# Performance work log

Hardware: AMD Instinct MI355X
Metric: run time of the kernel (lower is better)

Reference implementation:

```python
import jax, jax.numpy as jnp
import numpy as np

L = 3          # num_layer
E_DIM = 64     # emb_dim
B = 4          # graphs per batch
N = 20000      # nodes per graph
E = 320000     # edges per graph
IN_DIM = 21    # raw node feature dim (Linear(21, emb_dim))
BN_EPS = 1e-5


def setup_inputs() -> dict:
    key = jax.random.key(0)
    ks = jax.random.split(key, 16)
    h2 = 2 * E_DIM
    inp = {
        "x": jax.random.normal(ks[0], (B, N, IN_DIM), dtype=jnp.float32),
        "edge_index": jax.random.randint(ks[1], (B, 2, E), 0, N, dtype=jnp.int64),
        "edge_attr": jax.random.normal(ks[2], (B, E, 1), dtype=jnp.float32),
        # layer-0 input node embedding Linear(21, emb)
        "inW": jax.random.normal(ks[3], (IN_DIM, E_DIM), dtype=jnp.float32) * 0.1,
        "inb": jnp.zeros((E_DIM,), dtype=jnp.float32),
        # per-layer edge encoder Linear(1, emb)
        "edgeW": jax.random.normal(ks[4], (L, 1, E_DIM), dtype=jnp.float32) * 0.1,
        "edgeb": jnp.zeros((L, E_DIM), dtype=jnp.float32),
        # per-layer MLP: Linear(2e,2e) -> BN(2e) -> ReLU -> Linear(2e,e)
        "W1": jax.random.normal(ks[5], (L, h2, h2), dtype=jnp.float32) * 0.05,
        "b1": jnp.zeros((L, h2), dtype=jnp.float32),
        "gamma": jnp.ones((L, h2), dtype=jnp.float32),
        "beta": jnp.zeros((L, h2), dtype=jnp.float32),
        "W2": jax.random.normal(ks[6], (L, h2, E_DIM), dtype=jnp.float32) * 0.05,
        "b2": jnp.zeros((L, E_DIM), dtype=jnp.float32),
    }
    return inp


def _batchnorm_train(h, g, b):
    # BatchNorm1d in training mode: per-graph stats over the node dim, biased var
    m = h.mean(axis=0)
    v = jnp.mean((h - m) ** 2, axis=0)
    return (h - m) * jax.lax.rsqrt(v + BN_EPS) * g + b


def _gin_layer(xg, eig, eag, W1l, b1l, gl, bel, W2l, b2l):
    # xg [N,e], eig [2,E], eag [E,e]
    x_j = xg[eig[0]]                                   # gather source nodes [E,e]
    msg = jnp.concatenate([x_j, eag], axis=-1)         # [E,2e]
    aggr = jax.ops.segment_sum(msg, eig[1], num_segments=N)  # scatter-add [N,2e]
    h = aggr @ W1l + b1l
    h = _batchnorm_train(h, gl, bel)
    h = jax.nn.relu(h)
    return h @ W2l + b2l                               # [N,e]


def reference(x, edge_index, edge_attr, inW, inb, edgeW, edgeb, W1, b1, gamma, beta, W2, b2):
    h = x
    for l in range(L):
        ea = edge_attr @ edgeW[l] + edgeb[l]           # [B,E,e] edge embeddings
        if l == 0:
            h = h @ inW + inb                          # [B,N,e]
        h = jax.vmap(_gin_layer, in_axes=(0, 0, 0, None, None, None, None, None, None))(
            h, edge_index, ea, W1[l], b1[l], gamma[l], beta[l], W2[l], b2[l])
        if l < L - 1:                                  # drop_ratio=0 -> dropout is identity
            h = jax.nn.relu(h)
    return h  # JK='last'
```

## Files before the change

kernel.cpp:

```cpp
#include <hip/hip_runtime.h>
#include <hip/hip_bf16.h>
#include <hip/hip_fp16.h>

#define NB 4
#define NN 20000
#define NE 320000
#define IND 21
#define ED 64
#define H2 128
#define CAP 48
#define NRANGE 32
#define RNODES 625
#define BINCAP 160
#define SCAP 11264
#define BN_EPS 1e-5f

typedef __attribute__((ext_vector_type(8))) short bf16x8;
typedef __attribute__((ext_vector_type(4))) float f32x4;

__device__ __forceinline__ short f2bf(float f) {
    unsigned u = __float_as_uint(f);
    u += 0x7fffu + ((u >> 16) & 1u);
    return (short)(u >> 16);
}

__device__ __forceinline__ void add8(float* ac, const uint4 rv) {
    const float2 f0 = __half22float2(*(const __half2*)&rv.x);
    const float2 f1 = __half22float2(*(const __half2*)&rv.y);
    const float2 f2 = __half22float2(*(const __half2*)&rv.z);
    const float2 f3 = __half22float2(*(const __half2*)&rv.w);
    ac[0] += f0.x; ac[1] += f0.y; ac[2] += f1.x; ac[3] += f1.y;
    ac[4] += f2.x; ac[5] += f2.y; ac[6] += f3.x; ac[7] += f3.y;
}


__global__ __launch_bounds__(256) void k_compact(
    const int* __restrict__ ei, const float* __restrict__ eattr,
    uint2* __restrict__ stage, int* __restrict__ rcnt)
{
    __shared__ uint2 bins[NRANGE][BINCAP];
    __shared__ int lcnt[NRANGE];
    __shared__ int lbase[NRANGE];
    const int b = blockIdx.y;
    const int e0 = blockIdx.x * 2048;
    const int tid = threadIdx.x;
    if (tid < NRANGE) lcnt[tid] = 0;
    __syncthreads();
    const int* srcp = ei + (size_t)b * 2 * NE;
    const int* dstp = srcp + NE;
    const float* ap = eattr + (size_t)b * NE;
    #pragma unroll
    for (int it = 0; it < 8; ++it) {
        const int e = e0 + it * 256 + tid;
        if (e < NE) {
            const int dst = dstp[e];
            const int src = srcp[e];
            const float a = ap[e];
            const int r = dst / RNODES;
            const unsigned lo = ((unsigned)src & 0xffffu) | (__float_as_uint(a) & 0xffff0000u);
            const int p = atomicAdd(&lcnt[r], 1);
            if (p < BINCAP) bins[r][p] = make_uint2(lo, (unsigned)dst);
        }
    }
    __syncthreads();
    if (tid < NRANGE) lbase[tid] = atomicAdd(&rcnt[b * NRANGE + tid], min(lcnt[tid], BINCAP));
    __syncthreads();
    for (int r = 0; r < NRANGE; ++r) {
        const int c = min(lcnt[r], BINCAP);
        uint2* dstg = stage + (size_t)(b * NRANGE + r) * SCAP + lbase[r];
        for (int i = tid; i < c; i += 256) dstg[i] = bins[r][i];
    }
}

__global__ __launch_bounds__(256) void k_scatter(
    const uint2* __restrict__ stage, const int* __restrict__ rcnt,
    int* __restrict__ cnt, unsigned int* __restrict__ bucket)
{
    const int b = blockIdx.x >> 5;
    const int g = blockIdx.x & 31;
    const int count = min(rcnt[b * NRANGE + g], SCAP);
    const uint2* st = stage + (size_t)(b * NRANGE + g) * SCAP;
    for (int idx = threadIdx.x; idx < count; idx += 256) {
        const uint2 rec = st[idx];
        const int node = b * NN + (int)rec.y;
        const int p = atomicAdd(&cnt[node], 1);
        if (p < CAP) bucket[(size_t)node * CAP + p] = rec.x;
    }
}

__global__ __launch_bounds__(256) void k_in(
    const float* __restrict__ x, const float* __restrict__ inW,
    const float* __restrict__ inb, __half* __restrict__ h)
{
    const int b = blockIdx.y;
    const int t = blockIdx.x * 256 + threadIdx.x;
    const int n = t >> 6;
    const int c = t & 63;
    if (n >= NN) return;
    const float* xr = x + ((size_t)b * NN + n) * IND;
    float acc = inb[c];
    #pragma unroll
    for (int k = 0; k < IND; ++k) acc += xr[k] * inW[k * ED + c];
    h[((size_t)b * NN + n) * ED + c] = __float2half(acc);
}

__global__ __launch_bounds__(256) void k_prep(
    const float* __restrict__ W1, const float* __restrict__ W2,
    const float* __restrict__ edgeW, const float* __restrict__ edgeb,
    short* __restrict__ W1T, short* __restrict__ W2T,
    float* __restrict__ uv_all, float* __restrict__ stats_all)
{
    const int l = blockIdx.x;
    const int tid = threadIdx.x;
    ((float4*)(stats_all + l * 1024))[tid] = make_float4(0.f, 0.f, 0.f, 0.f);
    for (int i = tid; i < H2 * ED; i += 256) {
        const int j = i >> 6, k = i & 63;
        W1T[l * 8192 + i] = f2bf(W1[(size_t)l * H2 * H2 + k * H2 + j]);
    }
    for (int i = tid; i < ED * H2; i += 256) {
        const int c = i >> 7, k = i & 127;
        W2T[l * 8192 + i] = f2bf(W2[(size_t)l * H2 * ED + k * ED + c]);
    }
    if (tid < H2) {
        float u = 0.f, v = 0.f;
        for (int k = 0; k < ED; ++k) {
            const float w = W1[(size_t)l * H2 * H2 + (ED + k) * H2 + tid];
            u += edgeW[l * ED + k] * w;
            v += edgeb[l * ED + k] * w;
        }
        uv_all[l * 256 + tid] = u;
        uv_all[l * 256 + H2 + tid] = v;
    }
}


__global__ __launch_bounds__(256) void k_aggr_stats(
    const __half* __restrict__ h, const unsigned int* __restrict__ bucket,
    const int* __restrict__ cnt_arr, const short* __restrict__ W1Tl,
    const float* __restrict__ b1l, const float* __restrict__ uv_l,
    short* __restrict__ aggr_bf, float* __restrict__ s_attr,
    float* __restrict__ stats_l, int write_sattr)
{
    __shared__ short w1t[H2 * 72];
    __shared__ short atb[32 * 72];
    __shared__ float sdl[32], ddl[32];
    __shared__ float uL[H2], vL[H2], bbL[H2];
    const int tid = threadIdx.x;
    const int g = blockIdx.x & 7;
    const int b = g >> 1;
    const int t = ((int)blockIdx.x >> 3) * 2 + (g & 1);
    if (t >= NN / 32) return;
    const int n0 = t * 32;

    for (int i = tid; i < 1024; i += 256)
        *(uint4*)&w1t[(i >> 3) * 72 + (i & 7) * 8] = ((const uint4*)W1Tl)[i];
    if (tid < H2) { uL[tid] = uv_l[tid]; vL[tid] = uv_l[H2 + tid]; bbL[tid] = b1l[tid]; }

    {
        const int node = n0 + (tid >> 3);
        const int q = tid & 7;
        const int cntraw = cnt_arr[b * NN + node];
        const int cnt = min(cntraw, CAP);
        const unsigned int* row = bucket + (size_t)(b * NN + node) * CAP;
        const __half* hp = h + (size_t)b * NN * ED + q * 8;
        float ac[8];
        #pragma unroll
        for (int i = 0; i < 8; ++i) ac[i] = 0.f;
        float sa = 0.f;
        int j = 0;
        for (; j + 4 <= cnt; j += 4) {
            const uint4 ss = *(const uint4*)(row + j);
            const uint4 r0 = *(const uint4*)(hp + (size_t)(ss.x & 0xffffu) * ED);
            const uint4 r1 = *(const uint4*)(hp + (size_t)(ss.y & 0xffffu) * ED);
            const uint4 r2 = *(const uint4*)(hp + (size_t)(ss.z & 0xffffu) * ED);
            const uint4 r3 = *(const uint4*)(hp + (size_t)(ss.w & 0xffffu) * ED);
            sa += __uint_as_float(ss.x & 0xffff0000u) + __uint_as_float(ss.y & 0xffff0000u)
                + __uint_as_float(ss.z & 0xffff0000u) + __uint_as_float(ss.w & 0xffff0000u);
            add8(ac, r0); add8(ac, r1); add8(ac, r2); add8(ac, r3);
        }
        for (; j < cnt; ++j) {
            const unsigned e = row[j];
            sa += __uint_as_float(e & 0xffff0000u);
            const uint4 r0 = *(const uint4*)(hp + (size_t)(e & 0xffffu) * ED);
            add8(ac, r0);
        }
        uint4 pk;
        pk.x = (unsigned short)f2bf(ac[0]) | ((unsigned int)(unsigned short)f2bf(ac[1]) << 16);
        pk.y = (unsigned short)f2bf(ac[2]) | ((unsigned int)(unsigned short)f2bf(ac[3]) << 16);
        pk.z = (unsigned short)f2bf(ac[4]) | ((unsigned int)(unsigned short)f2bf(ac[5]) << 16);
        pk.w = (unsigned short)f2bf(ac[6]) | ((unsigned int)(unsigned short)f2bf(ac[7]) << 16);
        *(uint4*)&atb[(tid >> 3) * 72 + q * 8] = pk;
        *(uint4*)&aggr_bf[((size_t)b * NN + node) * ED + q * 8] = pk;
        if (q == 0) {
            sdl[tid >> 3] = sa;
            ddl[tid >> 3] = (float)cntraw;
            if (write_sattr) s_attr[b * NN + node] = sa;
        }
    }
    __syncthreads();

    const int l = tid & 63;
    const int w = tid >> 6;
    const int m = l & 15, quad = l >> 4;
    const int mt = w & 1;
    const int jb = (w >> 1) * 4;
    f32x4 acc[4];
    #pragma unroll
    for (int i = 0; i < 4; ++i) acc[i] = (f32x4){0.f, 0.f, 0.f, 0.f};
    #pragma unroll
    for (int kc = 0; kc < 2; ++kc) {
        const bf16x8 fa = *(const bf16x8*)&atb[(mt * 16 + m) * 72 + kc * 32 + quad * 8];
        #pragma unroll
        for (int t2 = 0; t2 < 4; ++t2) {
            const bf16x8 fb = *(const bf16x8*)&w1t[((jb + t2) * 16 + m) * 72 + kc * 32 + quad * 8];
            acc[t2] = __builtin_amdgcn_mfma_f32_16x16x32_bf16(fa, fb, acc[t2], 0, 0, 0);
        }
    }
    float sa_r[4], dg_r[4];
    #pragma unroll
    for (int r = 0; r < 4; ++r) {
        const int row = mt * 16 + quad * 4 + r;
        sa_r[r] = sdl[row]; dg_r[r] = ddl[row];
    }
    #pragma unroll
    for (int t2 = 0; t2 < 4; ++t2) {
        const int j = (jb + t2) * 16 + m;
        const float u = uL[j], v = vL[j], bb = bbL[j];
        float ls = 0.f, lq = 0.f;
        #pragma unroll
        for (int r = 0; r < 4; ++r) {
            const float h1 = acc[t2][r] + sa_r[r] * u + dg_r[r] * v + bb;
            ls += h1; lq += h1 * h1;
        }
        ls += __shfl_xor(ls, 16); ls += __shfl_xor(ls, 32);
        lq += __shfl_xor(lq, 16); lq += __shfl_xor(lq, 32);
        if (l < 16) {
            atomicAdd(&stats_l[b * H2 + j], ls);
            atomicAdd(&stats_l[NB * H2 + b * H2 + j], lq);
        }
    }
}

__global__ __launch_bounds__(256) void k_mlp_out(
    const short* __restrict__ aggr_bf, const float* __restrict__ s_attr,
    const int* __restrict__ cnt_arr, const short* __restrict__ W1Tl,
    const short* __restrict__ W2Tl, const float* __restrict__ b1l,
    const float* __restrict__ uv_l, const float* __restrict__ stats_l,
    const float* __restrict__ gamma_l, const float* __restrict__ beta_l,
    const float* __restrict__ b2l, __half* __restrict__ outh,
    float* __restrict__ outf, int last)
{
    __shared__ short wt[H2 * 72];
    __shared__ short ab[64 * 72];
    __shared__ short pb[64 * 136];
    __shared__ float sdl[64], ddl[64];
    __shared__ float uL[H2], vL[H2], bbL[H2], scL[H2], shL[H2];
    const int tid = threadIdx.x;
    const int g = blockIdx.x & 7;
    const int b = g >> 1;
    const int t = ((int)blockIdx.x >> 3) * 2 + (g & 1);
    if (t >= (NN + 63) / 64) return;
    const int n0 = t * 64;

    for (int i = tid; i < 1024; i += 256)
        *(uint4*)&wt[(i >> 3) * 72 + (i & 7) * 8] = ((const uint4*)W1Tl)[i];
    for (int i = tid; i < 512; i += 256)
        *(uint4*)&ab[(i >> 3) * 72 + (i & 7) * 8] =
            ((const uint4*)(aggr_bf + ((size_t)b * NN + n0) * ED))[i];
    if (tid < 64) sdl[tid] = s_attr[b * NN + n0 + tid];
    else if (tid < 128) ddl[tid - 64] = (float)cnt_arr[b * NN + n0 + tid - 64];
    if (tid < H2) {
        const int j = tid;
        const float mm = stats_l[b * H2 + j] * (1.f / NN);
        const float var = fmaxf(stats_l[NB * H2 + b * H2 + j] * (1.f / NN) - mm * mm, 0.f);
        const float rs = rsqrtf(var + BN_EPS);
        const float sc = gamma_l[j] * rs;
        scL[j] = sc;
        shL[j] = beta_l[j] - mm * sc;
        uL[j] = uv_l[j]; vL[j] = uv_l[H2 + j]; bbL[j] = b1l[j];
    }
    __syncthreads();

    const int l = tid & 63;
    const int w = tid >> 6;
    const int m = l & 15, quad = l >> 4;
    {
        f32x4 acc[8];
        #pragma unroll
        for (int i = 0; i < 8; ++i) acc[i] = (f32x4){0.f, 0.f, 0.f, 0.f};
        #pragma unroll
        for (int kc = 0; kc < 2; ++kc) {
            const bf16x8 fa = *(const bf16x8*)&ab[(w * 16 + m) * 72 + kc * 32 + quad * 8];
            #pragma unroll
            for (int t2 = 0; t2 < 8; ++t2) {
                const bf16x8 fb = *(const bf16x8*)&wt[(t2 * 16 + m) * 72 + kc * 32 + quad * 8];
                acc[t2] = __builtin_amdgcn_mfma_f32_16x16x32_bf16(fa, fb, acc[t2], 0, 0, 0);
            }
        }
        float sa_r[4], dg_r[4];
        #pragma unroll
        for (int r = 0; r < 4; ++r) {
            const int row = w * 16 + quad * 4 + r;
            sa_r[r] = sdl[row]; dg_r[r] = ddl[row];
        }
        #pragma unroll
        for (int t2 = 0; t2 < 8; ++t2) {
            const int j = t2 * 16 + m;
            const float u = uL[j], v = vL[j], bb = bbL[j];
            const float sc = scL[j], sh = shL[j];
            #pragma unroll
            for (int r = 0; r < 4; ++r) {
                const float h1 = acc[t2][r] + sa_r[r] * u + dg_r[r] * v + bb;
                pb[(w * 16 + quad * 4 + r) * 136 + j] = f2bf(fmaxf(h1 * sc + sh, 0.f));
            }
        }
    }
    __syncthreads();
    for (int i = tid; i < 1024; i += 256)
        *(uint4*)&wt[(i >> 4) * 136 + (i & 15) * 8] = ((const uint4*)W2Tl)[i];
    __syncthreads();
    {
        f32x4 acc2[4];
        #pragma unroll
        for (int i = 0; i < 4; ++i) acc2[i] = (f32x4){0.f, 0.f, 0.f, 0.f};
        #pragma unroll
        for (int kc = 0; kc < 4; ++kc) {
            const bf16x8 fa = *(const bf16x8*)&pb[(w * 16 + m) * 136 + kc * 32 + quad * 8];
            #pragma unroll
            for (int t2 = 0; t2 < 4; ++t2) {
                const bf16x8 fb = *(const bf16x8*)&wt[(t2 * 16 + m) * 136 + kc * 32 + quad * 8];
                acc2[t2] = __builtin_amdgcn_mfma_f32_16x16x32_bf16(fa, fb, acc2[t2], 0, 0, 0);
            }
        }
        #pragma unroll
        for (int t2 = 0; t2 < 4; ++t2) {
            const int c = t2 * 16 + m;
            const float bb2 = b2l[c];
            #pragma unroll
            for (int r = 0; r < 4; ++r) {
                const int row = w * 16 + quad * 4 + r;
                const int n = n0 + row;
                if (n < NN) {
                    const size_t idx = ((size_t)b * NN + n) * ED + c;
                    float o = acc2[t2][r] + bb2;
                    if (last) outf[idx] = o;
                    else outh[idx] = __float2half(fmaxf(o, 0.f));
                }
            }
        }
    }
}


extern "C" void kernel_launch(void* const* d_in, const int* in_sizes, int n_in,
                              void* d_out, int out_size, void* d_ws, size_t ws_size,
                              hipStream_t stream) {
    const float* x     = (const float*)d_in[0];
    const int*   ei    = (const int*)d_in[1];
    const float* eattr = (const float*)d_in[2];
    const float* inW   = (const float*)d_in[3];
    const float* inb   = (const float*)d_in[4];
    const float* edgeW = (const float*)d_in[5];
    const float* edgeb = (const float*)d_in[6];
    const float* W1    = (const float*)d_in[7];
    const float* b1    = (const float*)d_in[8];
    const float* gamma = (const float*)d_in[9];
    const float* beta  = (const float*)d_in[10];
    const float* W2    = (const float*)d_in[11];
    const float* b2    = (const float*)d_in[12];
    float* out = (float*)d_out;

    float* s_attr = (float*)d_ws;
    int*   cnt    = (int*)(s_attr + NB * NN);
    int*   rcnt   = cnt + NB * NN;
    uint2* stage  = (uint2*)(rcnt + 128);
    unsigned int* bucket = (unsigned int*)(stage + (size_t)NB * NRANGE * SCAP);
    short* aggr_bf = (short*)(bucket + (size_t)NB * NN * CAP);
    __half* hh    = (__half*)(aggr_bf + (size_t)NB * NN * ED);
    short* W1T    = (short*)(hh + (size_t)NB * NN * ED);
    short* W2T    = W1T + 3 * 8192;
    float* uv_all = (float*)(W2T + 3 * 8192);
    float* stats  = uv_all + 3 * 256;

    hipMemsetAsync(cnt, 0, ((size_t)NB * NN + 128) * sizeof(int), stream);

    k_compact<<<dim3((NE + 2047) / 2048, NB), 256, 0, stream>>>(ei, eattr, stage, rcnt);
    k_scatter<<<NB * NRANGE, 256, 0, stream>>>(stage, rcnt, cnt, bucket);
    k_in<<<dim3(NN * ED / 256, NB), 256, 0, stream>>>(x, inW, inb, hh);
    k_prep<<<3, 256, 0, stream>>>(W1, W2, edgeW, edgeb, W1T, W2T, uv_all, stats);

    const int nblk1 = 8 * ((NN / 32 + 1) / 2);
    const int nblk2 = 8 * (((NN + 63) / 64 + 1) / 2);
    for (int l = 0; l < 3; ++l) {
        k_aggr_stats<<<nblk1, 256, 0, stream>>>(hh, bucket, cnt,
            W1T + l * 8192, b1 + l * H2, uv_all + l * 256,
            aggr_bf, s_attr, stats + l * 1024, (l == 0) ? 1 : 0);
        k_mlp_out<<<nblk2, 256, 0, stream>>>(aggr_bf, s_attr, cnt,
            W1T + l * 8192, W2T + l * 8192, b1 + l * H2, uv_all + l * 256,
            stats + l * 1024, gamma + l * H2, beta + l * H2, b2 + l * ED,
            hh, out, (l == 2) ? 1 : 0);
    }
}
```

Measured before the change: 372.7 us.

## Shrink aggregation tiles, split edge lists across threads, read weights directly from global

The aggregation kernel now handles 16 nodes per block instead of 32. It stages each block's bucket rows in shared memory and splits each node's edge list across two half-threads, which are combined with a shuffle. Both kernels stop staging W1/W2 (and aggr rows) in LDS and load MFMA fragments straight from global, removing the staging loops and one barrier. This raises parallelism and memory-level concurrency in the gather, but adds more blocks and repeated global weight reads that rely on the cache.

```diff
diff --git a/kernel.cpp b/kernel.cpp
--- a/kernel.cpp
+++ b/kernel.cpp
@@ -141,95 +141,105 @@
     short* __restrict__ aggr_bf, float* __restrict__ s_attr,
     float* __restrict__ stats_l, int write_sattr)
 {
-    __shared__ short w1t[H2 * 72];
-    __shared__ short atb[32 * 72];
-    __shared__ float sdl[32], ddl[32];
+    __shared__ unsigned int brow[16 * CAP];
+    __shared__ short atb[16 * 72];
+    __shared__ float sdl[16], ddl[16];
     __shared__ float uL[H2], vL[H2], bbL[H2];
     const int tid = threadIdx.x;
     const int g = blockIdx.x & 7;
     const int b = g >> 1;
     const int t = ((int)blockIdx.x >> 3) * 2 + (g & 1);
-    if (t >= NN / 32) return;
-    const int n0 = t * 32;
-
-    for (int i = tid; i < 1024; i += 256)
-        *(uint4*)&w1t[(i >> 3) * 72 + (i & 7) * 8] = ((const uint4*)W1Tl)[i];
+    const int n0 = t * 16;
+
+    const int l = tid & 63;
+    const int w = tid >> 6;
+    const int m = l & 15, quad = l >> 4;
+
+    bf16x8 fb[2][2];
+    #pragma unroll
+    for (int t2 = 0; t2 < 2; ++t2)
+        #pragma unroll
+        for (int kc = 0; kc < 2; ++kc)
+            fb[t2][kc] = *(const bf16x8*)&W1Tl[((w * 2 + t2) * 16 + m) * 64 + kc * 32 + quad * 8];
+
     if (tid < H2) { uL[tid] = uv_l[tid]; vL[tid] = uv_l[H2 + tid]; bbL[tid] = b1l[tid]; }
 
     {
-        const int node = n0 + (tid >> 3);
-        const int q = tid & 7;
-        const int cntraw = cnt_arr[b * NN + node];
+        const unsigned int* bsrc = bucket + (size_t)(b * NN + n0) * CAP;
+        #pragma unroll
+        for (int i = tid; i < 16 * CAP; i += 256) brow[i] = bsrc[i];
+    }
+    __syncthreads();
+
+    {
+        const int node = tid >> 4;
+        const int sub = tid & 15;
+        const int q = sub & 7, eh = sub >> 3;
+        const int cntraw = cnt_arr[b * NN + n0 + node];
         const int cnt = min(cntraw, CAP);
-        const unsigned int* row = bucket + (size_t)(b * NN + node) * CAP;
+        const int hcnt = (cnt + 1) >> 1;
+        const int j1 = eh ? cnt : hcnt;
+        const unsigned int* row = &brow[node * CAP];
         const __half* hp = h + (size_t)b * NN * ED + q * 8;
         float ac[8];
         #pragma unroll
         for (int i = 0; i < 8; ++i) ac[i] = 0.f;
         float sa = 0.f;
-        int j = 0;
-        for (; j + 4 <= cnt; j += 4) {
-            const uint4 ss = *(const uint4*)(row + j);
-            const uint4 r0 = *(const uint4*)(hp + (size_t)(ss.x & 0xffffu) * ED);
-            const uint4 r1 = *(const uint4*)(hp + (size_t)(ss.y & 0xffffu) * ED);
-            const uint4 r2 = *(const uint4*)(hp + (size_t)(ss.z & 0xffffu) * ED);
-            const uint4 r3 = *(const uint4*)(hp + (size_t)(ss.w & 0xffffu) * ED);
-            sa += __uint_as_float(ss.x & 0xffff0000u) + __uint_as_float(ss.y & 0xffff0000u)
-                + __uint_as_float(ss.z & 0xffff0000u) + __uint_as_float(ss.w & 0xffff0000u);
+        int j = eh ? hcnt : 0;
+        for (; j + 4 <= j1; j += 4) {
+            const unsigned e0 = row[j], e1 = row[j + 1], e2 = row[j + 2], e3 = row[j + 3];
+            const uint4 r0 = *(const uint4*)(hp + (size_t)(e0 & 0xffffu) * ED);
+            const uint4 r1 = *(const uint4*)(hp + (size_t)(e1 & 0xffffu) * ED);
+            const uint4 r2 = *(const uint4*)(hp + (size_t)(e2 & 0xffffu) * ED);
+            const uint4 r3 = *(const uint4*)(hp + (size_t)(e3 & 0xffffu) * ED);
+            sa += __uint_as_float(e0 & 0xffff0000u) + __uint_as_float(e1 & 0xffff0000u)
+                + __uint_as_float(e2 & 0xffff0000u) + __uint_as_float(e3 & 0xffff0000u);
             add8(ac, r0); add8(ac, r1); add8(ac, r2); add8(ac, r3);
         }
-        for (; j < cnt; ++j) {
+        for (; j < j1; ++j) {
             const unsigned e = row[j];
             sa += __uint_as_float(e & 0xffff0000u);
             const uint4 r0 = *(const uint4*)(hp + (size_t)(e & 0xffffu) * ED);
             add8(ac, r0);
         }
-        uint4 pk;
-        pk.x = (unsigned short)f2bf(ac[0]) | ((unsigned int)(unsigned short)f2bf(ac[1]) << 16);
-        pk.y = (unsigned short)f2bf(ac[2]) | ((unsigned int)(unsigned short)f2bf(ac[3]) << 16);
-        pk.z = (unsigned short)f2bf(ac[4]) | ((unsigned int)(unsigned short)f2bf(ac[5]) << 16);
-        pk.w = (unsigned short)f2bf(ac[6]) | ((unsigned int)(unsigned short)f2bf(ac[7]) << 16);
-        *(uint4*)&atb[(tid >> 3) * 72 + q * 8] = pk;
-        *(uint4*)&aggr_bf[((size_t)b * NN + node) * ED + q * 8] = pk;
-        if (q == 0) {
-            sdl[tid >> 3] = sa;
-            ddl[tid >> 3] = (float)cntraw;
-            if (write_sattr) s_attr[b * NN + node] = sa;
-        }
-    }
-    __syncthreads();
-
-    const int l = tid & 63;
-    const int w = tid >> 6;
-    const int m = l & 15, quad = l >> 4;
-    const int mt = w & 1;
-    const int jb = (w >> 1) * 4;
-    f32x4 acc[4];
-    #pragma unroll
-    for (int i = 0; i < 4; ++i) acc[i] = (f32x4){0.f, 0.f, 0.f, 0.f};
+        #pragma unroll
+        for (int i = 0; i < 8; ++i) ac[i] += __shfl_xor(ac[i], 8);
+        sa += __shfl_xor(sa, 8);
+        if (eh == 0) {
+            uint4 pk;
+            pk.x = (unsigned short)f2bf(ac[0]) | ((unsigned int)(unsigned short)f2bf(ac[1]) << 16);
+            pk.y = (unsigned short)f2bf(ac[2]) | ((unsigned int)(unsigned short)f2bf(ac[3]) << 16);
+            pk.z = (unsigned short)f2bf(ac[4]) | ((unsigned int)(unsigned short)f2bf(ac[5]) << 16);
+            pk.w = (unsigned short)f2bf(ac[6]) | ((unsigned int)(unsigned short)f2bf(ac[7]) << 16);
+            *(uint4*)&atb[node * 72 + q * 8] = pk;
+            *(uint4*)&aggr_bf[((size_t)b * NN + n0 + node) * ED + q * 8] = pk;
+        }
+        if (sub == 0) {
+            sdl[node] = sa;
+            ddl[node] = (float)cntraw;
+            if (write_sattr) s_attr[b * NN + n0 + node] = sa;
+        }
+    }
+    __syncthreads();
+
+    f32x4 acc0 = {0.f, 0.f, 0.f, 0.f}, acc1 = {0.f, 0.f, 0.f, 0.f};
     #pragma unroll
     for (int kc = 0; kc < 2; ++kc) {
-        const bf16x8 fa = *(const bf16x8*)&atb[(mt * 16 + m) * 72 + kc * 32 + quad * 8];
-        #pragma unroll
-        for (int t2 = 0; t2 < 4; ++t2) {
-            const bf16x8 fb = *(const bf16x8*)&w1t[((jb + t2) * 16 + m) * 72 + kc * 32 + quad * 8];
-            acc[t2] = __builtin_amdgcn_mfma_f32_16x16x32_bf16(fa, fb, acc[t2], 0, 0, 0);
-        }
+        const bf16x8 fa = *(const bf16x8*)&atb[m * 72 + kc * 32 + quad * 8];
+        acc0 = __builtin_amdgcn_mfma_f32_16x16x32_bf16(fa, fb[0][kc], acc0, 0, 0, 0);
+        acc1 = __builtin_amdgcn_mfma_f32_16x16x32_bf16(fa, fb[1][kc], acc1, 0, 0, 0);
     }
     float sa_r[4], dg_r[4];
     #pragma unroll
-    for (int r = 0; r < 4; ++r) {
-        const int row = mt * 16 + quad * 4 + r;
-        sa_r[r] = sdl[row]; dg_r[r] = ddl[row];
-    }
-    #pragma unroll
-    for (int t2 = 0; t2 < 4; ++t2) {
-        const int j = (jb + t2) * 16 + m;
+    for (int r = 0; r < 4; ++r) { sa_r[r] = sdl[quad * 4 + r]; dg_r[r] = ddl[quad * 4 + r]; }
+    #pragma unroll
+    for (int t2 = 0; t2 < 2; ++t2) {
+        const int j = (w * 2 + t2) * 16 + m;
         const float u = uL[j], v = vL[j], bb = bbL[j];
         float ls = 0.f, lq = 0.f;
         #pragma unroll
         for (int r = 0; r < 4; ++r) {
-            const float h1 = acc[t2][r] + sa_r[r] * u + dg_r[r] * v + bb;
+            const float h1 = (t2 ? acc1[r] : acc0[r]) + sa_r[r] * u + dg_r[r] * v + bb;
             ls += h1; lq += h1 * h1;
         }
         ls += __shfl_xor(ls, 16); ls += __shfl_xor(ls, 32);
@@ -250,8 +260,6 @@
     const float* __restrict__ b2l, __half* __restrict__ outh,
     float* __restrict__ outf, int last)
 {
-    __shared__ short wt[H2 * 72];
-    __shared__ short ab[64 * 72];
     __shared__ short pb[64 * 136];
     __shared__ float sdl[64], ddl[64];
     __shared__ float uL[H2], vL[H2], bbL[H2], scL[H2], shL[H2];
@@ -262,13 +270,12 @@
     if (t >= (NN + 63) / 64) return;
     const int n0 = t * 64;
 
-    for (int i = tid; i < 1024; i += 256)
-        *(uint4*)&wt[(i >> 3) * 72 + (i & 7) * 8] = ((const uint4*)W1Tl)[i];
-    for (int i = tid; i < 512; i += 256)
-        *(uint4*)&ab[(i >> 3) * 72 + (i & 7) * 8] =
-            ((const uint4*)(aggr_bf + ((size_t)b * NN + n0) * ED))[i];
-    if (tid < 64) sdl[tid] = s_attr[b * NN + n0 + tid];
-    else if (tid < 128) ddl[tid - 64] = (float)cnt_arr[b * NN + n0 + tid - 64];
+    const int l = tid & 63;
+    const int w = tid >> 6;
+    const int m = l & 15, quad = l >> 4;
+
+    if (tid < 64) sdl[tid] = s_attr[b * NN + min(n0 + tid, NN - 1)];
+    else if (tid < 128) ddl[tid - 64] = (float)cnt_arr[b * NN + min(n0 + tid - 64, NN - 1)];
     if (tid < H2) {
         const int j = tid;
         const float mm = stats_l[b * H2 + j] * (1.f / NN);
@@ -279,22 +286,24 @@
         shL[j] = beta_l[j] - mm * sc;
         uL[j] = uv_l[j]; vL[j] = uv_l[H2 + j]; bbL[j] = b1l[j];
     }
-    __syncthreads();
-
-    const int l = tid & 63;
-    const int w = tid >> 6;
-    const int m = l & 15, quad = l >> 4;
+
+    const int rn = min(n0 + w * 16 + m, NN - 1);
+    bf16x8 fa1[2];
+    #pragma unroll
+    for (int kc = 0; kc < 2; ++kc)
+        fa1[kc] = *(const bf16x8*)&aggr_bf[((size_t)b * NN + rn) * ED + kc * 32 + quad * 8];
+    __syncthreads();
+
     {
         f32x4 acc[8];
         #pragma unroll
         for (int i = 0; i < 8; ++i) acc[i] = (f32x4){0.f, 0.f, 0.f, 0.f};
         #pragma unroll
-        for (int kc = 0; kc < 2; ++kc) {
-            const bf16x8 fa = *(const bf16x8*)&ab[(w * 16 + m) * 72 + kc * 32 + quad * 8];
+        for (int t2 = 0; t2 < 8; ++t2) {
             #pragma unroll
-            for (int t2 = 0; t2 < 8; ++t2) {
-                const bf16x8 fb = *(const bf16x8*)&wt[(t2 * 16 + m) * 72 + kc * 32 + quad * 8];
-                acc[t2] = __builtin_amdgcn_mfma_f32_16x16x32_bf16(fa, fb, acc[t2], 0, 0, 0);
+            for (int kc = 0; kc < 2; ++kc) {
+                const bf16x8 fbw = *(const bf16x8*)&W1Tl[(t2 * 16 + m) * 64 + kc * 32 + quad * 8];
+                acc[t2] = __builtin_amdgcn_mfma_f32_16x16x32_bf16(fa1[kc], fbw, acc[t2], 0, 0, 0);
             }
         }
         float sa_r[4], dg_r[4];
@@ -316,9 +325,6 @@
         }
     }
     __syncthreads();
-    for (int i = tid; i < 1024; i += 256)
-        *(uint4*)&wt[(i >> 4) * 136 + (i & 15) * 8] = ((const uint4*)W2Tl)[i];
-    __syncthreads();
     {
         f32x4 acc2[4];
         #pragma unroll
@@ -328,8 +334,8 @@
             const bf16x8 fa = *(const bf16x8*)&pb[(w * 16 + m) * 136 + kc * 32 + quad * 8];
             #pragma unroll
             for (int t2 = 0; t2 < 4; ++t2) {
-                const bf16x8 fb = *(const bf16x8*)&wt[(t2 * 16 + m) * 136 + kc * 32 + quad * 8];
-                acc2[t2] = __builtin_amdgcn_mfma_f32_16x16x32_bf16(fa, fb, acc2[t2], 0, 0, 0);
+                const bf16x8 fbw = *(const bf16x8*)&W2Tl[(t2 * 16 + m) * 128 + kc * 32 + quad * 8];
+                acc2[t2] = __builtin_amdgcn_mfma_f32_16x16x32_bf16(fa, fbw, acc2[t2], 0, 0, 0);
             }
         }
         #pragma unroll
@@ -389,7 +395,7 @@
     k_in<<<dim3(NN * ED / 256, NB), 256, 0, stream>>>(x, inW, inb, hh);
     k_prep<<<3, 256, 0, stream>>>(W1, W2, edgeW, edgeb, W1T, W2T, uv_all, stats);
 
-    const int nblk1 = 8 * ((NN / 32 + 1) / 2);
+    const int nblk1 = NB * (NN / 16);
     const int nblk2 = 8 * (((NN + 63) / 64 + 1) / 2);
     for (int l = 0; l < 3; ++l) {
         k_aggr_stats<<<nblk1, 256, 0, stream>>>(hh, bucket, cnt,
```

After: 399.6 us. +7.2%, slower.

## Fuse per-layer aggregation and MLP kernels into one persistent kernel with grid barriers

Applied to the files above, without the earlier changes.

Replaces the six per-layer launches (aggregate+stats, then MLP+output) with a single persistent kernel of 500 blocks that loops over the three layers and syncs with a spin-based grid barrier. Each block keeps its first-GEMM accumulators for five 32-node tiles in registers across the barrier. This removes the aggr_bf and s_attr round trips through global memory, the recomputation of the first GEMM, and the launch gaps. In exchange it adds a spin barrier that relies on all 500 blocks being resident at once, and much higher register pressure from the 80-float accumulator array, which could spill or limit occupancy.

```diff
diff --git a/kernel.cpp b/kernel.cpp
--- a/kernel.cpp
+++ b/kernel.cpp
@@ -13,6 +13,8 @@
 #define RNODES 625
 #define BINCAP 160
 #define SCAP 11264
+#define NBLK 500
+#define TPB 5
 #define BN_EPS 1e-5f
 
 typedef __attribute__((ext_vector_type(8))) short bf16x8;
@@ -31,6 +33,21 @@
     const float2 f3 = __half22float2(*(const __half2*)&rv.w);
     ac[0] += f0.x; ac[1] += f0.y; ac[2] += f1.x; ac[3] += f1.y;
     ac[4] += f2.x; ac[5] += f2.y; ac[6] += f3.x; ac[7] += f3.y;
+}
+
+__device__ __forceinline__ void gridbar(int* bar, int slot) {
+    __threadfence();
+    __syncthreads();
+    if (threadIdx.x == 0) {
+        atomicAdd(&bar[slot], 1);
+        int it = 0;
+        while (atomicAdd(&bar[slot], 0) < NBLK && it < (1 << 24)) {
+            ++it;
+            __builtin_amdgcn_s_sleep(8);
+        }
+    }
+    __syncthreads();
+    __threadfence();
 }
 
 
@@ -133,221 +150,204 @@
     }
 }
 
-
-__global__ __launch_bounds__(256) void k_aggr_stats(
-    const __half* __restrict__ h, const unsigned int* __restrict__ bucket,
-    const int* __restrict__ cnt_arr, const short* __restrict__ W1Tl,
-    const float* __restrict__ b1l, const float* __restrict__ uv_l,
-    short* __restrict__ aggr_bf, float* __restrict__ s_attr,
-    float* __restrict__ stats_l, int write_sattr)
-{
-    __shared__ short w1t[H2 * 72];
+__global__ __launch_bounds__(256, 2) void k_layers(
+    __half* __restrict__ hh, const unsigned int* __restrict__ bucket,
+    const int* __restrict__ cnt_arr, const short* __restrict__ W1T,
+    const short* __restrict__ W2T, const float* __restrict__ b1,
+    const float* __restrict__ uv_all, float* __restrict__ stats_all,
+    const float* __restrict__ gamma, const float* __restrict__ beta,
+    const float* __restrict__ b2, float* __restrict__ outf,
+    int* __restrict__ bar)
+{
+    __shared__ short wbuf[9216];
     __shared__ short atb[32 * 72];
-    __shared__ float sdl[32], ddl[32];
-    __shared__ float uL[H2], vL[H2], bbL[H2];
+    __shared__ short pb[32 * 136];
+    __shared__ float sdd[TPB][64];
+    __shared__ float uL[H2], vL[H2], bbL[H2], scL[H2], shL[H2];
     const int tid = threadIdx.x;
-    const int g = blockIdx.x & 7;
-    const int b = g >> 1;
-    const int t = ((int)blockIdx.x >> 3) * 2 + (g & 1);
-    if (t >= NN / 32) return;
-    const int n0 = t * 32;
-
-    for (int i = tid; i < 1024; i += 256)
-        *(uint4*)&w1t[(i >> 3) * 72 + (i & 7) * 8] = ((const uint4*)W1Tl)[i];
-    if (tid < H2) { uL[tid] = uv_l[tid]; vL[tid] = uv_l[H2 + tid]; bbL[tid] = b1l[tid]; }
-
-    {
-        const int node = n0 + (tid >> 3);
-        const int q = tid & 7;
-        const int cntraw = cnt_arr[b * NN + node];
-        const int cnt = min(cntraw, CAP);
-        const unsigned int* row = bucket + (size_t)(b * NN + node) * CAP;
-        const __half* hp = h + (size_t)b * NN * ED + q * 8;
-        float ac[8];
-        #pragma unroll
-        for (int i = 0; i < 8; ++i) ac[i] = 0.f;
-        float sa = 0.f;
-        int j = 0;
-        for (; j + 4 <= cnt; j += 4) {
-            const uint4 ss = *(const uint4*)(row + j);
-            const uint4 r0 = *(const uint4*)(hp + (size_t)(ss.x & 0xffffu) * ED);
-            const uint4 r1 = *(const uint4*)(hp + (size_t)(ss.y & 0xffffu) * ED);
-            const uint4 r2 = *(const uint4*)(hp + (size_t)(ss.z & 0xffffu) * ED);
-            const uint4 r3 = *(const uint4*)(hp + (size_t)(ss.w & 0xffffu) * ED);
-            sa += __uint_as_float(ss.x & 0xffff0000u) + __uint_as_float(ss.y & 0xffff0000u)
-                + __uint_as_float(ss.z & 0xffff0000u) + __uint_as_float(ss.w & 0xffff0000u);
-            add8(ac, r0); add8(ac, r1); add8(ac, r2); add8(ac, r3);
-        }
-        for (; j < cnt; ++j) {
-            const unsigned e = row[j];
-            sa += __uint_as_float(e & 0xffff0000u);
-            const uint4 r0 = *(const uint4*)(hp + (size_t)(e & 0xffffu) * ED);
-            add8(ac, r0);
-        }
-        uint4 pk;
-        pk.x = (unsigned short)f2bf(ac[0]) | ((unsigned int)(unsigned short)f2bf(ac[1]) << 16);
-        pk.y = (unsigned short)f2bf(ac[2]) | ((unsigned int)(unsigned short)f2bf(ac[3]) << 16);
-        pk.z = (unsigned short)f2bf(ac[4]) | ((unsigned int)(unsigned short)f2bf(ac[5]) << 16);
-        pk.w = (unsigned short)f2bf(ac[6]) | ((unsigned int)(unsigned short)f2bf(ac[7]) << 16);
-        *(uint4*)&atb[(tid >> 3) * 72 + q * 8] = pk;
-        *(uint4*)&aggr_bf[((size_t)b * NN + node) * ED + q * 8] = pk;
-        if (q == 0) {
-            sdl[tid >> 3] = sa;
-            ddl[tid >> 3] = (float)cntraw;
-            if (write_sattr) s_attr[b * NN + node] = sa;
-        }
-    }
-    __syncthreads();
-
-    const int l = tid & 63;
+    const int blk = blockIdx.x;
+    const int l0 = tid & 63;
     const int w = tid >> 6;
-    const int m = l & 15, quad = l >> 4;
+    const int m = l0 & 15, quad = l0 >> 4;
     const int mt = w & 1;
     const int jb = (w >> 1) * 4;
-    f32x4 acc[4];
-    #pragma unroll
-    for (int i = 0; i < 4; ++i) acc[i] = (f32x4){0.f, 0.f, 0.f, 0.f};
-    #pragma unroll
-    for (int kc = 0; kc < 2; ++kc) {
-        const bf16x8 fa = *(const bf16x8*)&atb[(mt * 16 + m) * 72 + kc * 32 + quad * 8];
+
+    f32x4 acc5[TPB][4];
+
+    for (int l = 0; l < 3; ++l) {
+        const short* W1Tl = W1T + l * 8192;
+        const float* uv_l = uv_all + l * 256;
+        float* stats_l = stats_all + l * 1024;
+
+        for (int i = tid; i < 1024; i += 256)
+            *(uint4*)&wbuf[(i >> 3) * 72 + (i & 7) * 8] = ((const uint4*)W1Tl)[i];
+        if (tid < H2) { uL[tid] = uv_l[tid]; vL[tid] = uv_l[H2 + tid]; bbL[tid] = b1[l * H2 + tid]; }
+        __syncthreads();
+
         #pragma unroll
-        for (int t2 = 0; t2 < 4; ++t2) {
-            const bf16x8 fb = *(const bf16x8*)&w1t[((jb + t2) * 16 + m) * 72 + kc * 32 + quad * 8];
-            acc[t2] = __builtin_amdgcn_mfma_f32_16x16x32_bf16(fa, fb, acc[t2], 0, 0, 0);
-        }
-    }
-    float sa_r[4], dg_r[4];
-    #pragma unroll
-    for (int r = 0; r < 4; ++r) {
-        const int row = mt * 16 + quad * 4 + r;
-        sa_r[r] = sdl[row]; dg_r[r] = ddl[row];
-    }
-    #pragma unroll
-    for (int t2 = 0; t2 < 4; ++t2) {
-        const int j = (jb + t2) * 16 + m;
-        const float u = uL[j], v = vL[j], bb = bbL[j];
-        float ls = 0.f, lq = 0.f;
+        for (int tt = 0; tt < TPB; ++tt) {
+            const int tile = blk * TPB + tt;
+            const int b = tile / 625;
+            const int n0 = (tile % 625) * 32;
+            {
+                const int node = n0 + (tid >> 3);
+                const int q = tid & 7;
+                const int cntraw = cnt_arr[b * NN + node];
+                const int cnt = min(cntraw, CAP);
+                const unsigned int* row = bucket + (size_t)(b * NN + node) * CAP;
+                const __half* hp = hh + (size_t)b * NN * ED + q * 8;
+                float ac[8];
+                #pragma unroll
+                for (int i = 0; i < 8; ++i) ac[i] = 0.f;
+                float sa = 0.f;
+                int j = 0;
+                for (; j + 4 <= cnt; j += 4) {
+                    const uint4 ss = *(const uint4*)(row + j);
+                    const uint4 r0 = *(const uint4*)(hp + (size_t)(ss.x & 0xffffu) * ED);
+                    const uint4 r1 = *(const uint4*)(hp + (size_t)(ss.y & 0xffffu) * ED);
+                    const uint4 r2 = *(const uint4*)(hp + (size_t)(ss.z & 0xffffu) * ED);
+                    const uint4 r3 = *(const uint4*)(hp + (size_t)(ss.w & 0xffffu) * ED);
+                    sa += __uint_as_float(ss.x & 0xffff0000u) + __uint_as_float(ss.y & 0xffff0000u)
+                        + __uint_as_float(ss.z & 0xffff0000u) + __uint_as_float(ss.w & 0xffff0000u);
+                    add8(ac, r0); add8(ac, r1); add8(ac, r2); add8(ac, r3);
+                }
+                for (; j < cnt; ++j) {
+                    const unsigned e = row[j];
+                    sa += __uint_as_float(e & 0xffff0000u);
+                    const uint4 r0 = *(const uint4*)(hp + (size_t)(e & 0xffffu) * ED);
+                    add8(ac, r0);
+                }
+                uint4 pk;
+                pk.x = (unsigned short)f2bf(ac[0]) | ((unsigned int)(unsigned short)f2bf(ac[1]) << 16);
+                pk.y = (unsigned short)f2bf(ac[2]) | ((unsigned int)(unsigned short)f2bf(ac[3]) << 16);
+                pk.z = (unsigned short)f2bf(ac[4]) | ((unsigned int)(unsigned short)f2bf(ac[5]) << 16);
+                pk.w = (unsigned short)f2bf(ac[6]) | ((unsigned int)(unsigned short)f2bf(ac[7]) << 16);
+                *(uint4*)&atb[(tid >> 3) * 72 + q * 8] = pk;
+                if (q == 0) {
+                    sdd[tt][(tid >> 3) * 2] = sa;
+                    sdd[tt][(tid >> 3) * 2 + 1] = (float)cntraw;
+                }
+            }
+            __syncthreads();
+            #pragma unroll
+            for (int i = 0; i < 4; ++i) acc5[tt][i] = (f32x4){0.f, 0.f, 0.f, 0.f};
+            #pragma unroll
+            for (int kc = 0; kc < 2; ++kc) {
+                const bf16x8 fa = *(const bf16x8*)&atb[(mt * 16 + m) * 72 + kc * 32 + quad * 8];
+                #pragma unroll
+                for (int t2 = 0; t2 < 4; ++t2) {
+                    const bf16x8 fb = *(const bf16x8*)&wbuf[((jb + t2) * 16 + m) * 72 + kc * 32 + quad * 8];
+                    acc5[tt][t2] = __builtin_amdgcn_mfma_f32_16x16x32_bf16(fa, fb, acc5[tt][t2], 0, 0, 0);
+                }
+            }
+            float sa_r[4], dg_r[4];
+            #pragma unroll
+            for (int r = 0; r < 4; ++r) {
+                const int row = mt * 16 + quad * 4 + r;
+                sa_r[r] = sdd[tt][row * 2]; dg_r[r] = sdd[tt][row * 2 + 1];
+            }
+            #pragma unroll
+            for (int t2 = 0; t2 < 4; ++t2) {
+                const int j = (jb + t2) * 16 + m;
+                const float u = uL[j], v = vL[j], bb = bbL[j];
+                float ls = 0.f, lq = 0.f;
+                #pragma unroll
+                for (int r = 0; r < 4; ++r) {
+                    const float h1 = acc5[tt][t2][r] + sa_r[r] * u + dg_r[r] * v + bb;
+                    ls += h1; lq += h1 * h1;
+                }
+                ls += __shfl_xor(ls, 16); ls += __shfl_xor(ls, 32);
+                lq += __shfl_xor(lq, 16); lq += __shfl_xor(lq, 32);
+                if (l0 < 16) {
+                    atomicAdd(&stats_l[b * H2 + j], ls);
+                    atomicAdd(&stats_l[NB * H2 + b * H2 + j], lq);
+                }
+            }
+            __syncthreads();
+        }
+
+        gridbar(bar, l * 2);
+
+        {
+            const short* W2Tl = W2T + l * 8192;
+            for (int i = tid; i < 1024; i += 256)
+                *(uint4*)&wbuf[(i >> 4) * 136 + (i & 15) * 8] = ((const uint4*)W2Tl)[i];
+        }
+        if (tid < H2) {
+            const int j = tid;
+            #pragma unroll
+            for (int b = 0; b < NB; ++b) {
+            }
+        }
+        __syncthreads();
+        const int last = (l == 2);
         #pragma unroll
-        for (int r = 0; r < 4; ++r) {
-            const float h1 = acc[t2][r] + sa_r[r] * u + dg_r[r] * v + bb;
-            ls += h1; lq += h1 * h1;
-        }
-        ls += __shfl_xor(ls, 16); ls += __shfl_xor(ls, 32);
-        lq += __shfl_xor(lq, 16); lq += __shfl_xor(lq, 32);
-        if (l < 16) {
-            atomicAdd(&stats_l[b * H2 + j], ls);
-            atomicAdd(&stats_l[NB * H2 + b * H2 + j], lq);
-        }
-    }
-}
-
-__global__ __launch_bounds__(256) void k_mlp_out(
-    const short* __restrict__ aggr_bf, const float* __restrict__ s_attr,
-    const int* __restrict__ cnt_arr, const short* __restrict__ W1Tl,
-    const short* __restrict__ W2Tl, const float* __restrict__ b1l,
-    const float* __restrict__ uv_l, const float* __restrict__ stats_l,
-    const float* __restrict__ gamma_l, const float* __restrict__ beta_l,
-    const float* __restrict__ b2l, __half* __restrict__ outh,
-    float* __restrict__ outf, int last)
-{
-    __shared__ short wt[H2 * 72];
-    __shared__ short ab[64 * 72];
-    __shared__ short pb[64 * 136];
-    __shared__ float sdl[64], ddl[64];
-    __shared__ float uL[H2], vL[H2], bbL[H2], scL[H2], shL[H2];
-    const int tid = threadIdx.x;
-    const int g = blockIdx.x & 7;
-    const int b = g >> 1;
-    const int t = ((int)blockIdx.x >> 3) * 2 + (g & 1);
-    if (t >= (NN + 63) / 64) return;
-    const int n0 = t * 64;
-
-    for (int i = tid; i < 1024; i += 256)
-        *(uint4*)&wt[(i >> 3) * 72 + (i & 7) * 8] = ((const uint4*)W1Tl)[i];
-    for (int i = tid; i < 512; i += 256)
-        *(uint4*)&ab[(i >> 3) * 72 + (i & 7) * 8] =
-            ((const uint4*)(aggr_bf + ((size_t)b * NN + n0) * ED))[i];
-    if (tid < 64) sdl[tid] = s_attr[b * NN + n0 + tid];
-    else if (tid < 128) ddl[tid - 64] = (float)cnt_arr[b * NN + n0 + tid - 64];
-    if (tid < H2) {
-        const int j = tid;
-        const float mm = stats_l[b * H2 + j] * (1.f / NN);
-        const float var = fmaxf(stats_l[NB * H2 + b * H2 + j] * (1.f / NN) - mm * mm, 0.f);
-        const float rs = rsqrtf(var + BN_EPS);
-        const float sc = gamma_l[j] * rs;
-        scL[j] = sc;
-        shL[j] = beta_l[j] - mm * sc;
-        uL[j] = uv_l[j]; vL[j] = uv_l[H2 + j]; bbL[j] = b1l[j];
-    }
-    __syncthreads();
-
-    const int l = tid & 63;
-    const int w = tid >> 6;
-    const int m = l & 15, quad = l >> 4;
-    {
-        f32x4 acc[8];
-        #pragma unroll
-        for (int i = 0; i < 8; ++i) acc[i] = (f32x4){0.f, 0.f, 0.f, 0.f};
-        #pragma unroll
-        for (int kc = 0; kc < 2; ++kc) {
-            const bf16x8 fa = *(const bf16x8*)&ab[(w * 16 + m) * 72 + kc * 32 + quad * 8];
-            #pragma unroll
-            for (int t2 = 0; t2 < 8; ++t2) {
-                const bf16x8 fb = *(const bf16x8*)&wt[(t2 * 16 + m) * 72 + kc * 32 + quad * 8];
-                acc[t2] = __builtin_amdgcn_mfma_f32_16x16x32_bf16(fa, fb, acc[t2], 0, 0, 0);
-            }
-        }
-        float sa_r[4], dg_r[4];
-        #pragma unroll
-        for (int r = 0; r < 4; ++r) {
-            const int row = w * 16 + quad * 4 + r;
-            sa_r[r] = sdl[row]; dg_r[r] = ddl[row];
-        }
-        #pragma unroll
-        for (int t2 = 0; t2 < 8; ++t2) {
-            const int j = t2 * 16 + m;
-            const float u = uL[j], v = vL[j], bb = bbL[j];
-            const float sc = scL[j], sh = shL[j];
-            #pragma unroll
-            for (int r = 0; r < 4; ++r) {
-                const float h1 = acc[t2][r] + sa_r[r] * u + dg_r[r] * v + bb;
-                pb[(w * 16 + quad * 4 + r) * 136 + j] = f2bf(fmaxf(h1 * sc + sh, 0.f));
-            }
-        }
-    }
-    __syncthreads();
-    for (int i = tid; i < 1024; i += 256)
-        *(uint4*)&wt[(i >> 4) * 136 + (i & 15) * 8] = ((const uint4*)W2Tl)[i];
-    __syncthreads();
-    {
-        f32x4 acc2[4];
-        #pragma unroll
-        for (int i = 0; i < 4; ++i) acc2[i] = (f32x4){0.f, 0.f, 0.f, 0.f};
-        #pragma unroll
-        for (int kc = 0; kc < 4; ++kc) {
-            const bf16x8 fa = *(const bf16x8*)&pb[(w * 16 + m) * 136 + kc * 32 + quad * 8];
-            #pragma unroll
-            for (int t2 = 0; t2 < 4; ++t2) {
-                const bf16x8 fb = *(const bf16x8*)&wt[(t2 * 16 + m) * 136 + kc * 32 + quad * 8];
-                acc2[t2] = __builtin_amdgcn_mfma_f32_16x16x32_bf16(fa, fb, acc2[t2], 0, 0, 0);
-            }
-        }
-        #pragma unroll
-        for (int t2 = 0; t2 < 4; ++t2) {
-            const int c = t2 * 16 + m;
-            const float bb2 = b2l[c];
-            #pragma unroll
-            for (int r = 0; r < 4; ++r) {
-                const int row = w * 16 + quad * 4 + r;
-                const int n = n0 + row;
-                if (n < NN) {
-                    const size_t idx = ((size_t)b * NN + n) * ED + c;
-                    float o = acc2[t2][r] + bb2;
-                    if (last) outf[idx] = o;
-                    else outh[idx] = __float2half(fmaxf(o, 0.f));
-                }
-            }
-        }
+        for (int tt = 0; tt < TPB; ++tt) {
+            const int tile = blk * TPB + tt;
+            const int b = tile / 625;
+            const int n0 = (tile % 625) * 32;
+            if (tid < H2) {
+                const int j = tid;
+                const float mm = stats_l[b * H2 + j] * (1.f / NN);
+                const float var = fmaxf(stats_l[NB * H2 + b * H2 + j] * (1.f / NN) - mm * mm, 0.f);
+                const float rs = rsqrtf(var + BN_EPS);
+                const float sc = gamma[l * H2 + j] * rs;
+                scL[j] = sc;
+                shL[j] = beta[l * H2 + j] - mm * sc;
+            }
+            __syncthreads();
+            {
+                float sa_r[4], dg_r[4];
+                #pragma unroll
+                for (int r = 0; r < 4; ++r) {
+                    const int row = mt * 16 + quad * 4 + r;
+                    sa_r[r] = sdd[tt][row * 2]; dg_r[r] = sdd[tt][row * 2 + 1];
+                }
+                #pragma unroll
+                for (int t2 = 0; t2 < 4; ++t2) {
+                    const int j = (jb + t2) * 16 + m;
+                    const float u = uL[j], v = vL[j], bb = bbL[j];
+                    const float sc = scL[j], sh = shL[j];
+                    #pragma unroll
+                    for (int r = 0; r < 4; ++r) {
+                        const float h1 = acc5[tt][t2][r] + sa_r[r] * u + dg_r[r] * v + bb;
+                        pb[(mt * 16 + quad * 4 + r) * 136 + j] = f2bf(fmaxf(h1 * sc + sh, 0.f));
+                    }
+                }
+            }
+            __syncthreads();
+            {
+                const int nb = (w >> 1) * 2;
+                f32x4 acc2[2];
+                acc2[0] = (f32x4){0.f, 0.f, 0.f, 0.f};
+                acc2[1] = (f32x4){0.f, 0.f, 0.f, 0.f};
+                #pragma unroll
+                for (int kc = 0; kc < 4; ++kc) {
+                    const bf16x8 fa = *(const bf16x8*)&pb[(mt * 16 + m) * 136 + kc * 32 + quad * 8];
+                    #pragma unroll
+                    for (int t2 = 0; t2 < 2; ++t2) {
+                        const bf16x8 fb = *(const bf16x8*)&wbuf[((nb + t2) * 16 + m) * 136 + kc * 32 + quad * 8];
+                        acc2[t2] = __builtin_amdgcn_mfma_f32_16x16x32_bf16(fa, fb, acc2[t2], 0, 0, 0);
+                    }
+                }
+                #pragma unroll
+                for (int t2 = 0; t2 < 2; ++t2) {
+                    const int c = (nb + t2) * 16 + m;
+                    const float bb2 = b2[l * ED + c];
+                    #pragma unroll
+                    for (int r = 0; r < 4; ++r) {
+                        const int row = mt * 16 + quad * 4 + r;
+                        const size_t idx = ((size_t)b * NN + n0 + row) * ED + c;
+                        float o = acc2[t2][r] + bb2;
+                        if (last) outf[idx] = o;
+                        else hh[idx] = __float2half(fmaxf(o, 0.f));
+                    }
+                }
+            }
+            __syncthreads();
+        }
+
+        if (l < 2) gridbar(bar, l * 2 + 1);
     }
 }
 
@@ -370,34 +370,24 @@
     const float* b2    = (const float*)d_in[12];
     float* out = (float*)d_out;
 
-    float* s_attr = (float*)d_ws;
-    int*   cnt    = (int*)(s_attr + NB * NN);
+    int*   cnt    = (int*)d_ws;
     int*   rcnt   = cnt + NB * NN;
-    uint2* stage  = (uint2*)(rcnt + 128);
+    int*   bar    = rcnt + 128;
+    uint2* stage  = (uint2*)(bar + 8);
     unsigned int* bucket = (unsigned int*)(stage + (size_t)NB * NRANGE * SCAP);
-    short* aggr_bf = (short*)(bucket + (size_t)NB * NN * CAP);
-    __half* hh    = (__half*)(aggr_bf + (size_t)NB * NN * ED);
+    __half* hh    = (__half*)(bucket + (size_t)NB * NN * CAP);
     short* W1T    = (short*)(hh + (size_t)NB * NN * ED);
     short* W2T    = W1T + 3 * 8192;
     float* uv_all = (float*)(W2T + 3 * 8192);
     float* stats  = uv_all + 3 * 256;
 
-    hipMemsetAsync(cnt, 0, ((size_t)NB * NN + 128) * sizeof(int), stream);
+    hipMemsetAsync(cnt, 0, ((size_t)NB * NN + 136) * sizeof(int), stream);
 
     k_compact<<<dim3((NE + 2047) / 2048, NB), 256, 0, stream>>>(ei, eattr, stage, rcnt);
     k_scatter<<<NB * NRANGE, 256, 0, stream>>>(stage, rcnt, cnt, bucket);
     k_in<<<dim3(NN * ED / 256, NB), 256, 0, stream>>>(x, inW, inb, hh);
     k_prep<<<3, 256, 0, stream>>>(W1, W2, edgeW, edgeb, W1T, W2T, uv_all, stats);
 
-    const int nblk1 = 8 * ((NN / 32 + 1) / 2);
-    const int nblk2 = 8 * (((NN + 63) / 64 + 1) / 2);
-    for (int l = 0; l < 3; ++l) {
-        k_aggr_stats<<<nblk1, 256, 0, stream>>>(hh, bucket, cnt,
-            W1T + l * 8192, b1 + l * H2, uv_all + l * 256,
-            aggr_bf, s_attr, stats + l * 1024, (l == 0) ? 1 : 0);
-        k_mlp_out<<<nblk2, 256, 0, stream>>>(aggr_bf, s_attr, cnt,
-            W1T + l * 8192, W2T + l * 8192, b1 + l * H2, uv_all + l * 256,
-            stats + l * 1024, gamma + l * H2, beta + l * H2, b2 + l * ED,
-            hh, out, (l == 2) ? 1 : 0);
-    }
-}
+    k_layers<<<NBLK, 256, 0, stream>>>(hh, bucket, cnt, W1T, W2T, b1,
+                                       uv_all, stats, gamma, beta, b2, out, bar);
+}
```

Result: slower. 1.008 ms (+170.4%).
